# Kernel optimization log

Hardware: AMD Instinct MI355X
Metric: run time of the kernel (lower is better)

Reference implementation:

```python
import jax, jax.numpy as jnp
import numpy as np

B, S, D = 2, 4096, 1152
H = 16
HD = D // H  # 72
SCALE = HD ** -0.5


def setup_inputs() -> dict:
    key = jax.random.key(0)
    ks = jax.random.split(key, 9)
    std = 1.0 / np.sqrt(D)
    return {
        "x": jax.random.normal(ks[0], (B, S, D), dtype=jnp.float32),
        "q_w": jax.random.normal(ks[1], (D, D), dtype=jnp.float32) * std,
        "q_b": jax.random.normal(ks[2], (D,), dtype=jnp.float32) * std,
        "k_w": jax.random.normal(ks[3], (D, D), dtype=jnp.float32) * std,
        "k_b": jax.random.normal(ks[4], (D,), dtype=jnp.float32) * std,
        "v_w": jax.random.normal(ks[5], (D, D), dtype=jnp.float32) * std,
        "v_b": jax.random.normal(ks[6], (D,), dtype=jnp.float32) * std,
        "o_w": jax.random.normal(ks[7], (D, D), dtype=jnp.float32) * std,
        "o_b": jax.random.normal(ks[8], (D,), dtype=jnp.float32) * std,
    }


def reference(x, q_w, q_b, k_w, k_b, v_w, v_b, o_w, o_b):
    # Linear layers: torch nn.Linear stores weight as [out, in]; y = x @ W^T + b
    q = jnp.einsum("bsd,ed->bse", x, q_w) + q_b
    k = jnp.einsum("bsd,ed->bse", x, k_w) + k_b
    v = jnp.einsum("bsd,ed->bse", x, v_w) + v_b
    # [B, H, S, HD]
    q = q.reshape(B, S, H, HD).transpose(0, 2, 1, 3)
    k = k.reshape(B, S, H, HD).transpose(0, 2, 1, 3)
    v = v.reshape(B, S, H, HD).transpose(0, 2, 1, 3)
    # scores [B, H, S, S]
    scores = jnp.einsum("bhqd,bhkd->bhqk", q, k) * SCALE
    attn = jax.nn.softmax(scores.astype(jnp.float32), axis=-1).astype(q.dtype)
    out = jnp.einsum("bhqk,bhkd->bhqd", attn, v)
    out = out.transpose(0, 2, 1, 3).reshape(B, S, D)
    return jnp.einsum("bsd,ed->bse", out, o_w) + o_b
```

## Files before the change

kernel.cpp:

```cpp
#include <hip/hip_runtime.h>

#define NB 2
#define NS 4096
#define ND 1152
#define NH 16
#define HD 72
#define HP 80
#define VP 96
#define QSCALE (0.11785113019775793f * 1.4426950408889634f)

typedef float f32x4 __attribute__((ext_vector_type(4)));
typedef float f32x16 __attribute__((ext_vector_type(16)));
typedef __bf16 bf16x8 __attribute__((ext_vector_type(8)));
typedef unsigned short u16x8 __attribute__((ext_vector_type(8)));
typedef unsigned short u16x4 __attribute__((ext_vector_type(4)));
typedef unsigned int u32x4 __attribute__((ext_vector_type(4)));

__device__ __forceinline__ unsigned short f2bf(float f) {
  return __builtin_bit_cast(unsigned short, (__bf16)f);
}
__device__ __forceinline__ bf16x8 asbf(u16x8 u) {
  return __builtin_bit_cast(bf16x8, u);
}
__device__ __forceinline__ unsigned cvtpk(float lo, float hi) {
  unsigned d;
  asm("v_cvt_pk_bf16_f32 %0, %1, %2" : "=v"(d) : "v"(lo), "v"(hi));
  return d;
}
__device__ __forceinline__ void lane32swap(unsigned &x, unsigned &y) {
  asm volatile("v_permlane32_swap_b32 %0, %1" : "+v"(x), "+v"(y));
}
#if __has_builtin(__builtin_amdgcn_exp2f)
#define EXP2(x) __builtin_amdgcn_exp2f(x)
#else
#define EXP2(x) exp2f(x)
#endif
__device__ __forceinline__ void gll16(const void* g, void* l) {
  __builtin_amdgcn_global_load_lds(
      (__attribute__((address_space(1))) void*)(unsigned long long)g,
      (__attribute__((address_space(3))) void*)l, 16, 0, 0);
}

__global__ __launch_bounds__(256) void cvt_pad(
    const float* __restrict__ x,
    const float* __restrict__ qw, const float* __restrict__ kw,
    const float* __restrict__ vw,
    unsigned short* __restrict__ xb, unsigned short* __restrict__ wb,
    unsigned short* __restrict__ q80, unsigned short* __restrict__ k80,
    unsigned short* __restrict__ vt) {
  if (blockIdx.x < 6552) {
    const size_t NX = (size_t)8192 * ND;
    const size_t NW = (size_t)ND * ND;
    size_t i = ((size_t)blockIdx.x * 256 + threadIdx.x) * 8;
    const float* s; unsigned short* d; size_t off;
    if (i < NX)            { s = x;  d = xb;          off = i; }
    else if (i < NX + NW)  { s = qw; d = wb;          off = i - NX; }
    else if (i < NX + 2*NW){ s = kw; d = wb + NW;     off = i - NX - NW; }
    else                   { s = vw; d = wb + 2 * NW; off = i - NX - 2 * NW; }
    f32x4 a = *(const f32x4*)(s + off);
    f32x4 b = *(const f32x4*)(s + off + 4);
    u16x8 o;
#pragma unroll
    for (int j = 0; j < 4; ++j) { o[j] = f2bf(a[j]); o[j + 4] = f2bf(b[j]); }
    *(u16x8*)(d + off) = o;
  } else {
    int i = (blockIdx.x - 6552) * 256 + threadIdx.x;
    u16x8 z = {};
    if (i < 131072) {
      *(u16x8*)(q80 + (size_t)i * HP + HD) = z;
    } else if (i < 262144) {
      *(u16x8*)(k80 + (size_t)(i - 131072) * HP + HD) = z;
    } else {
      int j = i - 262144;
      int bh = j / 12288;
      int r = j % 12288;
      int row = 72 + r / 512;
      int col = (r % 512) * 8;
      u16x8 v = z;
      if (row == HD) {
#pragma unroll
        for (int j8 = 0; j8 < 8; ++j8) v[j8] = 0x3F80;
      }
      *(u16x8*)(vt + ((size_t)bh * VP + row) * NS + col) = v;
    }
  }
}

__global__ __launch_bounds__(256) void qkv_gemm(
    const unsigned short* __restrict__ xb, const unsigned short* __restrict__ wb,
    const float* __restrict__ qbias, const float* __restrict__ kbias,
    const float* __restrict__ vbias,
    unsigned short* __restrict__ qp, unsigned short* __restrict__ kp,
    unsigned short* __restrict__ vt)
{
  const int mb = blockIdx.x * 128;
  const int nb = blockIdx.y * 128;
  const int proj = blockIdx.z;
  const unsigned short* w = wb + (size_t)proj * (ND * ND);

  __shared__ __align__(16) unsigned short la[128 * 64];
  __shared__ __align__(16) unsigned short lb[128 * 64];

  const int t = threadIdx.x;
  const int lane = t & 63;
  const int wid = t >> 6;
  const int mo = (wid >> 1) * 64, no = (wid & 1) * 64;
  const int l15 = lane & 15, l4 = lane >> 4;

  const unsigned short* ga = xb + (size_t)(mb + wid * 32 + (lane >> 3)) * ND + (lane & 7) * 8;
  const unsigned short* gb = w  + (size_t)(nb + wid * 32 + (lane >> 3)) * ND + (lane & 7) * 8;

  f32x4 acc[4][4] = {};

  if (proj < 2) {
    const float* bias = proj == 0 ? qbias : kbias;
    for (int kt = 0; kt < ND / 64; ++kt) {
      const int k0 = kt * 64;
      __syncthreads();
#pragma unroll
      for (int j = 0; j < 4; ++j) {
        gll16(ga + (size_t)j * 8 * ND + k0, &la[(wid * 4 + j) * 512]);
        gll16(gb + (size_t)j * 8 * ND + k0, &lb[(wid * 4 + j) * 512]);
      }
      __syncthreads();
#pragma unroll
      for (int ks = 0; ks < 2; ++ks) {
        bf16x8 af[4], bfr[4];
#pragma unroll
        for (int mt = 0; mt < 4; ++mt)
          af[mt] = asbf(*(const u16x8*)(&la[(mo + mt * 16 + l15) * 64 + ks * 32 + l4 * 8]));
#pragma unroll
        for (int nt = 0; nt < 4; ++nt)
          bfr[nt] = asbf(*(const u16x8*)(&lb[(no + nt * 16 + l15) * 64 + ks * 32 + l4 * 8]));
#pragma unroll
        for (int mt = 0; mt < 4; ++mt)
#pragma unroll
          for (int nt = 0; nt < 4; ++nt)
            acc[mt][nt] = __builtin_amdgcn_mfma_f32_16x16x32_bf16(af[mt], bfr[nt], acc[mt][nt], 0, 0, 0);
      }
    }

#pragma unroll
    for (int mt = 0; mt < 4; ++mt) {
#pragma unroll
      for (int nt = 0; nt < 4; ++nt) {
        const int n = nb + no + nt * 16 + l15;
        const float bval = bias[n];
        const int h = n / HD, hd = n % HD;
#pragma unroll
        for (int r = 0; r < 4; ++r) {
          const int m = mb + mo + mt * 16 + l4 * 4 + r;
          const int b = m >> 12, sl = m & (NS - 1);
          const int bh = b * NH + h;
          float v = acc[mt][nt][r] + bval;
          if (proj == 0)
            qp[((size_t)bh * NS + sl) * HP + hd] = f2bf(v * QSCALE);
          else
            kp[((size_t)bh * NS + sl) * HP + hd] = f2bf(v);
        }
      }
    }
  } else {
    for (int kt = 0; kt < ND / 64; ++kt) {
      const int k0 = kt * 64;
      __syncthreads();
#pragma unroll
      for (int j = 0; j < 4; ++j) {
        gll16(ga + (size_t)j * 8 * ND + k0, &la[(wid * 4 + j) * 512]);
        gll16(gb + (size_t)j * 8 * ND + k0, &lb[(wid * 4 + j) * 512]);
      }
      __syncthreads();
#pragma unroll
      for (int ks = 0; ks < 2; ++ks) {
        bf16x8 af[4], bfr[4];
#pragma unroll
        for (int mt = 0; mt < 4; ++mt)
          af[mt] = asbf(*(const u16x8*)(&la[(mo + mt * 16 + l15) * 64 + ks * 32 + l4 * 8]));
#pragma unroll
        for (int nt = 0; nt < 4; ++nt)
          bfr[nt] = asbf(*(const u16x8*)(&lb[(no + nt * 16 + l15) * 64 + ks * 32 + l4 * 8]));
#pragma unroll
        for (int mt = 0; mt < 4; ++mt)
#pragma unroll
          for (int nt = 0; nt < 4; ++nt)
            acc[mt][nt] = __builtin_amdgcn_mfma_f32_16x16x32_bf16(bfr[nt], af[mt], acc[mt][nt], 0, 0, 0);
      }
    }

#pragma unroll
    for (int mt = 0; mt < 4; ++mt) {
      const int m = mb + mo + mt * 16 + l15;
      const int b = m >> 12, sl = m & (NS - 1);
#pragma unroll
      for (int nt = 0; nt < 4; ++nt) {
#pragma unroll
        for (int r = 0; r < 4; ++r) {
          const int n = nb + no + nt * 16 + l4 * 4 + r;
          const int h = n / HD, hd = n % HD;
          vt[(((size_t)(b * NH + h)) * VP + hd) * NS + sl] =
              f2bf(acc[mt][nt][r] + vbias[n]);
        }
      }
    }
  }
}

__device__ __forceinline__ void softmax_pv(f32x16 s, const unsigned short* cur,
                                           int mt, int lane, f32x16 o[3]) {
#pragma unroll
  for (int i = 0; i < 16; ++i) s[i] = EXP2(s[i]);
  unsigned dk[8];
#pragma unroll
  for (int r2 = 0; r2 < 4; ++r2) {
    dk[2 * r2]     = cvtpk(s[4 * r2],     s[4 * r2 + 1]);
    dk[2 * r2 + 1] = cvtpk(s[4 * r2 + 2], s[4 * r2 + 3]);
  }
#pragma unroll
  for (int a = 0; a < 2; ++a) {
    unsigned x0 = dk[4 * a + 0], y0 = dk[4 * a + 2];
    unsigned x1 = dk[4 * a + 1], y1 = dk[4 * a + 3];
    lane32swap(x0, y0);
    lane32swap(x1, y1);
    u32x4 wd = {x0, x1, y0, y1};
    bf16x8 pf = __builtin_bit_cast(bf16x8, wd);
    const int ks2 = mt * 2 + a;
    __builtin_amdgcn_s_setprio(1);
#pragma unroll
    for (int hdt = 0; hdt < 3; ++hdt) {
      bf16x8 vf = asbf(*(const u16x8*)(&cur[(640 + (hdt * 4 + ks2) * 64 + lane) * 8]));
      o[hdt] = __builtin_amdgcn_mfma_f32_32x32x16_bf16(vf, pf, o[hdt], 0, 0, 0);
    }
    __builtin_amdgcn_s_setprio(0);
  }
}

__global__ __launch_bounds__(512, 4) void attn_fwd(
    const unsigned short* __restrict__ qp,
    const unsigned short* __restrict__ kp,
    const unsigned short* __restrict__ vt,
    unsigned short* __restrict__ ao,
    const float* __restrict__ ow, unsigned short* __restrict__ owb)
{
  if (blockIdx.x >= 512) {
    const int tid = (blockIdx.x - 512) * 512 + threadIdx.x;
    for (size_t c = tid; c < (size_t)ND * ND / 8; c += 8192) {
      size_t off = c * 8;
      f32x4 a = *(const f32x4*)(ow + off);
      f32x4 b = *(const f32x4*)(ow + off + 4);
      u16x8 o;
#pragma unroll
      for (int j = 0; j < 4; ++j) { o[j] = f2bf(a[j]); o[j + 4] = f2bf(b[j]); }
      *(u16x8*)(owb + off) = o;
    }
    return;
  }

  const int d = blockIdx.x;
  const int qt = (d >> 3) & 15;
  const int bh = (d & 7) + 8 * (d >> 7);
  const int b = bh >> 4, h = bh & 15;
  const int qs0 = qt * 256;

  __shared__ __align__(16) unsigned short sm[2 * 1408 * 8];

  const int t = threadIdx.x;
  const int wv = t >> 6;
  const int lane = t & 63;
  const int q = lane & 31;
  const int hh = lane >> 5;

  bf16x8 qf[5];
  {
    const unsigned short* qrow =
        qp + ((size_t)bh * NS + qs0 + wv * 32 + q) * HP + hh * 8;
#pragma unroll
    for (int ks = 0; ks < 5; ++ks)
      qf[ks] = asbf(*(const u16x8*)(qrow + ks * 16));
  }

  const unsigned short* kb0 = kp + (size_t)bh * NS * HP;
  const unsigned short* vb0 = vt + (size_t)bh * VP * NS;
  const unsigned short* gp[3];
  int stp[3], goff[3];
  const bool has2 = wv < 6;
#pragma unroll
  for (int j = 0; j < 3; ++j) {
    int g = wv + 8 * j;
    if (g > 21) g = 21;
    if (g < 10) {
      gp[j] = kb0 + ((g / 5) * 32 + (lane & 31)) * HP + (g % 5) * 16 + (lane >> 5) * 8;
      stp[j] = 64 * HP;
    } else {
      const int f = g - 10;
      gp[j] = vb0 + (size_t)((f >> 2) * 32 + (lane & 31)) * NS + (f & 3) * 16 + (lane >> 5) * 8;
      stp[j] = 64;
    }
    goff[j] = g * 512;
  }

  f32x16 o[3] = {};

  gll16(gp[0], sm + goff[0]); gp[0] += stp[0];
  gll16(gp[1], sm + goff[1]); gp[1] += stp[1];
  if (has2) { gll16(gp[2], sm + goff[2]); gp[2] += stp[2]; }
  __syncthreads();

  for (int it = 0; it < NS / 64; ++it) {
    unsigned short* cur = sm + (it & 1) * 11264;
    unsigned short* nxt = sm + ((it + 1) & 1) * 11264;
    if (it < NS / 64 - 1) {
      gll16(gp[0], nxt + goff[0]); gp[0] += stp[0];
      gll16(gp[1], nxt + goff[1]); gp[1] += stp[1];
      if (has2) { gll16(gp[2], nxt + goff[2]); gp[2] += stp[2]; }
    }

#pragma unroll
    for (int mt = 0; mt < 2; ++mt) {
      f32x16 s = {};
      __builtin_amdgcn_s_setprio(1);
#pragma unroll
      for (int ks = 0; ks < 5; ++ks) {
        bf16x8 kf = asbf(*(const u16x8*)(&cur[((mt * 5 + ks) * 64 + lane) * 8]));
        s = __builtin_amdgcn_mfma_f32_32x32x16_bf16(kf, qf[ks], s, 0, 0, 0);
      }
      __builtin_amdgcn_s_setprio(0);
      softmax_pv(s, cur, mt, lane, o);
    }
    __syncthreads();
  }

  const float l_tot = __shfl(o[2][4], q);
  const float inv = 1.0f / l_tot;
  const int srow = qs0 + wv * 32 + q;
  unsigned short* ob = ao + ((size_t)b * NS + srow) * ND + h * HD;
#pragma unroll
  for (int hdt = 0; hdt < 3; ++hdt)
#pragma unroll
    for (int r2 = 0; r2 < 4; ++r2) {
      const int hd0 = hdt * 32 + r2 * 8 + hh * 4;
      if (hd0 < HD) {
        u16x4 ov;
#pragma unroll
        for (int r0 = 0; r0 < 4; ++r0) ov[r0] = f2bf(o[hdt][r2 * 4 + r0] * inv);
        *(u16x4*)(ob + hd0) = ov;
      }
    }
}

__global__ __launch_bounds__(256) void oproj_gemm(
    const unsigned short* __restrict__ a,
    const unsigned short* __restrict__ wbf, const float* __restrict__ bias,
    float* __restrict__ out)
{
  const int mb = blockIdx.x * 128;
  const int nb = blockIdx.y * 128;

  __shared__ __align__(16) unsigned short la[128 * 64];
  __shared__ __align__(16) unsigned short lb[128 * 64];

  const int t = threadIdx.x;
  const int lane = t & 63;
  const int wid = t >> 6;
  const int mo = (wid >> 1) * 64, no = (wid & 1) * 64;
  const int l15 = lane & 15, l4 = lane >> 4;

  const unsigned short* ga = a   + (size_t)(mb + wid * 32 + (lane >> 3)) * ND + (lane & 7) * 8;
  const unsigned short* gb = wbf + (size_t)(nb + wid * 32 + (lane >> 3)) * ND + (lane & 7) * 8;

  f32x4 acc[4][4] = {};

  for (int kt = 0; kt < ND / 64; ++kt) {
    const int k0 = kt * 64;
    __syncthreads();
#pragma unroll
    for (int j = 0; j < 4; ++j) {
      gll16(ga + (size_t)j * 8 * ND + k0, &la[(wid * 4 + j) * 512]);
      gll16(gb + (size_t)j * 8 * ND + k0, &lb[(wid * 4 + j) * 512]);
    }
    __syncthreads();
#pragma unroll
    for (int ks = 0; ks < 2; ++ks) {
      bf16x8 af[4], bfr[4];
#pragma unroll
      for (int mt = 0; mt < 4; ++mt)
        af[mt] = asbf(*(const u16x8*)(&la[(mo + mt * 16 + l15) * 64 + ks * 32 + l4 * 8]));
#pragma unroll
      for (int nt = 0; nt < 4; ++nt)
        bfr[nt] = asbf(*(const u16x8*)(&lb[(no + nt * 16 + l15) * 64 + ks * 32 + l4 * 8]));
#pragma unroll
      for (int mt = 0; mt < 4; ++mt)
#pragma unroll
        for (int nt = 0; nt < 4; ++nt)
          acc[mt][nt] = __builtin_amdgcn_mfma_f32_16x16x32_bf16(af[mt], bfr[nt], acc[mt][nt], 0, 0, 0);
    }
  }

#pragma unroll
  for (int mt = 0; mt < 4; ++mt)
#pragma unroll
    for (int nt = 0; nt < 4; ++nt) {
      const int n = nb + no + nt * 16 + l15;
      const float bval = bias[n];
#pragma unroll
      for (int r = 0; r < 4; ++r) {
        const int m = mb + mo + mt * 16 + l4 * 4 + r;
        out[(size_t)m * ND + n] = acc[mt][nt][r] + bval;
      }
    }
}

extern "C" void kernel_launch(void* const* d_in, const int* in_sizes, int n_in,
                              void* d_out, int out_size, void* d_ws, size_t ws_size,
                              hipStream_t stream) {
  const float* x  = (const float*)d_in[0];
  const float* qw = (const float*)d_in[1];
  const float* qb = (const float*)d_in[2];
  const float* kw = (const float*)d_in[3];
  const float* kb = (const float*)d_in[4];
  const float* vw = (const float*)d_in[5];
  const float* vb = (const float*)d_in[6];
  const float* ow = (const float*)d_in[7];
  const float* ob = (const float*)d_in[8];
  float* out = (float*)d_out;

  char* ws = (char*)d_ws;
  unsigned short* q80    = (unsigned short*)(ws);
  unsigned short* k80    = (unsigned short*)(ws + 20971520);
  unsigned short* v_t    = (unsigned short*)(ws + 41943040);
  unsigned short* xb     = (unsigned short*)(ws + 67108864);
  unsigned short* wb     = (unsigned short*)(ws + 85983232);

  cvt_pad<<<dim3(9112), dim3(256), 0, stream>>>(x, qw, kw, vw, xb, wb,
                                                q80, k80, v_t);
  qkv_gemm<<<dim3(64, 9, 3), dim3(256), 0, stream>>>(xb, wb, qb, kb, vb,
                                                     q80, k80, v_t);
  attn_fwd<<<dim3(528), dim3(512), 0, stream>>>(q80, k80, v_t, xb ,
                                                ow, wb );
  oproj_gemm<<<dim3(64, 9), dim3(256), 0, stream>>>(xb , wb, ob, out);
}
```

Baseline: 331.4 us.

## Triple-buffer K/V shared-memory tiles with partial vmcnt waits

Moves the attention kernel's K/V LDS staging from double to triple buffering, so loads are issued two iterations ahead. Explicit s_waitcnt vmcnt with a partial count plus a raw s_barrier replace the full __syncthreads, letting the next tile's loads stay in flight across the barrier. This costs 50% more LDS per block, which may reduce occupancy. It also relies on hand-counted outstanding vector-memory operations being correct.

```diff
diff --git a/kernel.cpp b/kernel.cpp
--- a/kernel.cpp
+++ b/kernel.cpp
@@ -261,7 +261,7 @@
   const int b = bh >> 4, h = bh & 15;
   const int qs0 = qt * 256;
 
-  __shared__ __align__(16) unsigned short sm[2 * 1408 * 8];
+  __shared__ __align__(16) unsigned short sm[3 * 1408 * 8];
 
   const int t = threadIdx.x;
   const int wv = t >> 6;
@@ -300,20 +300,31 @@
 
   f32x16 o[3] = {};
 
-  gll16(gp[0], sm + goff[0]); gp[0] += stp[0];
-  gll16(gp[1], sm + goff[1]); gp[1] += stp[1];
-  if (has2) { gll16(gp[2], sm + goff[2]); gp[2] += stp[2]; }
-  __syncthreads();
+  unsigned short* bf0 = sm;
+  unsigned short* bf1 = sm + 11264;
+  unsigned short* bf2 = sm + 22528;
+
+  gll16(gp[0], bf0 + goff[0]);
+  gll16(gp[1], bf0 + goff[1]);
+  if (has2) gll16(gp[2], bf0 + goff[2]);
+  gp[0] += stp[0]; gp[1] += stp[1]; gp[2] += stp[2];
+  gll16(gp[0], bf1 + goff[0]);
+  gll16(gp[1], bf1 + goff[1]);
+  if (has2) gll16(gp[2], bf1 + goff[2]);
+  gp[0] += stp[0]; gp[1] += stp[1]; gp[2] += stp[2];
+  if (has2) asm volatile("s_waitcnt vmcnt(3)" ::: "memory");
+  else      asm volatile("s_waitcnt vmcnt(2)" ::: "memory");
+  __builtin_amdgcn_s_barrier();
 
   for (int it = 0; it < NS / 64; ++it) {
-    unsigned short* cur = sm + (it & 1) * 11264;
-    unsigned short* nxt = sm + ((it + 1) & 1) * 11264;
-    if (it < NS / 64 - 1) {
-      gll16(gp[0], nxt + goff[0]); gp[0] += stp[0];
-      gll16(gp[1], nxt + goff[1]); gp[1] += stp[1];
-      if (has2) { gll16(gp[2], nxt + goff[2]); gp[2] += stp[2]; }
-    }
-
+    if (it < NS / 64 - 2) {
+      gll16(gp[0], bf2 + goff[0]);
+      gll16(gp[1], bf2 + goff[1]);
+      if (has2) gll16(gp[2], bf2 + goff[2]);
+      gp[0] += stp[0]; gp[1] += stp[1]; gp[2] += stp[2];
+    }
+
+    const unsigned short* cur = bf0;
 #pragma unroll
     for (int mt = 0; mt < 2; ++mt) {
       f32x16 s = {};
@@ -326,7 +337,17 @@
       __builtin_amdgcn_s_setprio(0);
       softmax_pv(s, cur, mt, lane, o);
     }
-    __syncthreads();
+
+    if (it < NS / 64 - 1) {
+      if (it < NS / 64 - 2) {
+        if (has2) asm volatile("s_waitcnt vmcnt(3)" ::: "memory");
+        else      asm volatile("s_waitcnt vmcnt(2)" ::: "memory");
+      } else {
+        asm volatile("s_waitcnt vmcnt(0)" ::: "memory");
+      }
+      __builtin_amdgcn_s_barrier();
+      unsigned short* tmp = bf0; bf0 = bf1; bf1 = bf2; bf2 = tmp;
+    }
   }
 
   const float l_tot = __shfl(o[2][4], q);
```

Result: no change. 332.2 us (+0.2%).
